# Performance work log

Measured on AMD Instinct MI355X. Metric: run time of the kernel, lower is better.

Reference implementation:

```python
import jax, jax.numpy as jnp
import numpy as np

B, N, HID = 2, 2048, 1024
NH = 16
HD = HID // NH

def setup_inputs() -> dict:
    key = jax.random.key(0)
    ks = jax.random.split(key, 5)
    s = 0.02
    return {
        "hidden_states": jax.random.normal(ks[0], (B, N, HID), jnp.float32),
        "attention_mask": jnp.zeros((B, 1, 1, N), jnp.float32),
        "Wq": jax.random.normal(ks[1], (HID, HID), jnp.float32) * s,
        "bq": jnp.zeros((HID,), jnp.float32),
        "Wk": jax.random.normal(ks[2], (HID, HID), jnp.float32) * s,
        "bk": jnp.zeros((HID,), jnp.float32),
        "Wv": jax.random.normal(ks[3], (HID, HID), jnp.float32) * s,
        "bv": jnp.zeros((HID,), jnp.float32),
    }

def reference(hidden_states, attention_mask, Wq, bq, Wk, bk, Wv, bv):
    b, n, _ = hidden_states.shape
    def split_heads(t):  # [b,n,hid] -> [b,h,n,d]
        return t.reshape(b, n, NH, HD).transpose(0, 2, 1, 3)
    q = split_heads(hidden_states @ Wq.T + bq)
    k = split_heads(hidden_states @ Wk.T + bk)
    v = split_heads(hidden_states @ Wv.T + bv)
    scores = jnp.einsum('bhnd,bhmd->bhnm', q, k) / jnp.sqrt(jnp.float32(HD)).astype(q.dtype)
    scores = scores + attention_mask
    scores = jnp.maximum(scores, jnp.finfo(scores.dtype).min)
    probs = jax.nn.softmax(scores, axis=-1)
    out = jnp.einsum('bhnm,bhmd->bhnd', probs, v)
    return out.transpose(0, 2, 1, 3).reshape(b, n, NH * HD)
```

## Files before the change

kernel.cpp:

```cpp
#include <hip/hip_runtime.h>

typedef unsigned short u16;
typedef unsigned int   u32;
typedef __attribute__((ext_vector_type(8))) short bf16x8;
typedef __attribute__((ext_vector_type(4))) float f32x4;
typedef __attribute__((ext_vector_type(2))) unsigned int u32x2;

__device__ __forceinline__ float bf2f(u16 u) { return __uint_as_float(((u32)u) << 16); }
__device__ __forceinline__ u16 f2bf(float f) {
    return (u16)((__float_as_uint(f) + 0x8000u) >> 16);
}
__device__ __forceinline__ u32 cvt_pk_bf16(float lo, float hi) {
    u32 r;
    asm("v_cvt_pk_bf16_f32 %0, %1, %2" : "=v"(r) : "v"(lo), "v"(hi));
    return r;
}
__device__ __forceinline__ void gload16(const void* g, void* l) {
    __builtin_amdgcn_global_load_lds((const __attribute__((address_space(1))) void*)g,
                                     (__attribute__((address_space(3))) void*)l, 16, 0, 0);
}
#define VMCNT(n) asm volatile("s_waitcnt vmcnt(" #n ")" ::: "memory")

struct us4 { u16 x, y, z, w; };
__global__ void cvt_all(const float* __restrict__ hs, const float* __restrict__ wq,
                        const float* __restrict__ wk, const float* __restrict__ wv,
                        u16* __restrict__ dst)
{
    int i = blockIdx.x * blockDim.x + threadIdx.x;
    const int stride = gridDim.x * blockDim.x;
    us4* d4 = (us4*)dst;
    for (; i < 1835008; i += stride) {
        const float4* s4;
        int j = i;
        if (j < 1048576)      { s4 = (const float4*)hs; }
        else if (j < 1310720) { s4 = (const float4*)wq; j -= 1048576; }
        else if (j < 1572864) { s4 = (const float4*)wk; j -= 1310720; }
        else                  { s4 = (const float4*)wv; j -= 1572864; }
        float4 v = s4[j];
        us4 o;
        o.x = f2bf(v.x); o.y = f2bf(v.y); o.z = f2bf(v.z); o.w = f2bf(v.w);
        d4[i] = o;
    }
}

__global__ __launch_bounds__(256) void qkv_gemm(
    const u16* __restrict__ hs,
    const u16* __restrict__ Wq, const u16* __restrict__ Wk, const u16* __restrict__ Wv,
    const float* __restrict__ bq, const float* __restrict__ bk, const float* __restrict__ bv,
    u16* __restrict__ oq, u16* __restrict__ ok, u16* __restrict__ ovt)
{
    __shared__ u16 smem[18432];
    u16* sA = smem;
    u16* sB = smem + 8192;

    const int tid  = threadIdx.x;
    const int lane = tid & 63;
    const int w    = tid >> 6;
    const int c15  = lane & 15;
    const int q4   = lane >> 4;
    const int mat  = blockIdx.x >> 3;
    const int cb   = blockIdx.x & 7;
    const int rb   = blockIdx.y;
    const int wr   = w >> 1, wc = w & 1;

    const u16*   W    = (mat == 0) ? Wq : (mat == 1 ? Wk : Wv);
    const float* bias = (mat == 0) ? bq : (mat == 1 ? bk : bv);

    f32x4 acc[4][4] = {};

    const int rs = tid >> 3;
    const int cs = ((tid & 7) ^ (rs & 7)) * 8;
    const u16* gA = hs + (rb * 128) * 1024;
    const u16* gB = W + (cb * 128) * 1024;

    for (int kb = 0; kb < 1024; kb += 64) {
        __syncthreads();
#pragma unroll
        for (int p = 0; p < 4; ++p)
            gload16(gA + (rs + 32 * p) * 1024 + kb + cs, sA + p * 2048 + w * 512);
#pragma unroll
        for (int p = 0; p < 4; ++p)
            gload16(gB + (rs + 32 * p) * 1024 + kb + cs, sB + p * 2048 + w * 512);
        __syncthreads();

#pragma unroll
        for (int kk = 0; kk < 2; ++kk) {
            const int cpos = ((kk * 4 + q4) ^ (c15 & 7)) * 8;
            bf16x8 af[4], bf[4];
#pragma unroll
            for (int mt = 0; mt < 4; ++mt)
                af[mt] = *(const bf16x8*)(sA + (wr * 64 + mt * 16 + c15) * 64 + cpos);
#pragma unroll
            for (int nt = 0; nt < 4; ++nt)
                bf[nt] = *(const bf16x8*)(sB + (wc * 64 + nt * 16 + c15) * 64 + cpos);
#pragma unroll
            for (int mt = 0; mt < 4; ++mt)
#pragma unroll
                for (int nt = 0; nt < 4; ++nt)
                    acc[mt][nt] = __builtin_amdgcn_mfma_f32_16x16x32_bf16(
                        af[mt], bf[nt], acc[mt][nt], 0, 0, 0);
        }
    }

    __syncthreads();
    const int h = cb * 2 + wc;
    float bvv[4];
#pragma unroll
    for (int nt = 0; nt < 4; ++nt)
        bvv[nt] = bias[cb * 128 + wc * 64 + nt * 16 + c15];

    u16* sc = smem + w * 4608;
    if (mat != 2) {
        u16* dst = (mat == 0) ? oq : ok;
#pragma unroll
        for (int mt = 0; mt < 4; ++mt)
#pragma unroll
            for (int nt = 0; nt < 4; ++nt)
#pragma unroll
                for (int rr = 0; rr < 4; ++rr)
                    sc[(mt * 16 + q4 * 4 + rr) * 72 + nt * 16 + c15] =
                        f2bf(acc[mt][nt][rr] + bvv[nt]);
#pragma unroll
        for (int p = 0; p < 8; ++p) {
            const int s = p * 64 + lane;
            const int rl = s >> 3, oct = (s & 7) * 8;
            bf16x8 vv = *(const bf16x8*)(sc + rl * 72 + oct);
            const int n = rb * 128 + wr * 64 + rl;
            const int bb = n >> 11, nn = n & 2047;
            *(bf16x8*)(dst + (((bb * 16 + h) * 2048) + nn) * 64 + oct) = vv;
        }
    } else {
#pragma unroll
        for (int mt = 0; mt < 4; ++mt)
#pragma unroll
            for (int nt = 0; nt < 4; ++nt)
#pragma unroll
                for (int rr = 0; rr < 4; ++rr)
                    sc[(nt * 16 + c15) * 72 + mt * 16 + q4 * 4 + rr] =
                        f2bf(acc[mt][nt][rr] + bvv[nt]);
#pragma unroll
        for (int p = 0; p < 8; ++p) {
            const int s = p * 64 + lane;
            const int dr = s >> 3, noct = (s & 7) * 8;
            bf16x8 vv = *(const bf16x8*)(sc + dr * 72 + noct);
            const int n0 = rb * 128 + wr * 64 + noct;
            const int bb = n0 >> 11, nn = n0 & 2047;
            *(bf16x8*)(ovt + ((bb * 16 + h) * 64 + dr) * 2048 + nn) = vv;
        }
    }
}

__global__ __launch_bounds__(256, 2) void attn(
    const u16* __restrict__ qm, const u16* __restrict__ km, const u16* __restrict__ vtm,
    const float* __restrict__ mask, float* __restrict__ out)
{
    __shared__ u16 sK0[8192];
    __shared__ u16 sV0[8192];
    __shared__ u16 sK1[8192];
    __shared__ u16 sV1[8192];

    const int tid = threadIdx.x, lane = tid & 63, w = tid >> 6;
    const int c15 = lane & 15, q4 = lane >> 4;
    const int bh = blockIdx.x;
    const int qt = blockIdx.y;
    const int b = bh >> 4;

    bf16x8 qf[2][2];
    const u16* qbase = qm + (bh * 2048 + qt * 128 + w * 32) * 64;
#pragma unroll
    for (int rt = 0; rt < 2; ++rt)
#pragma unroll
        for (int kt = 0; kt < 2; ++kt)
            qf[rt][kt] = *(const bf16x8*)(qbase + (rt * 16 + c15) * 64 + kt * 32 + q4 * 8);

    float l_acc[2] = {0.f, 0.f};
    f32x4 accO[2][4] = {};

    const u16* kbase  = km  + bh * 2048 * 64;
    const u16* vtbase = vtm + bh * 64 * 2048;

    const int rK   = tid >> 3;
    const int colK = ((tid & 7) ^ (rK & 7)) * 8;
    const int prK  = (rK & 3) | ((rK & 0x0C) << 1) | ((rK & 0x10) >> 2);
    const int rV   = tid >> 4;
    const int colV = ((tid & 15) ^ (rV & 7)) * 8;
    const int ldsW = w * 512;

    const float* mbase = mask + b * 2048 + 8 * q4;

    auto stage = [&](u16* dK, u16* dV, int TT) {
        const u16* kg = kbase + TT * 128 * 64;
        const u16* vg = vtbase + TT * 128;
#pragma unroll
        for (int p = 0; p < 4; ++p)
            gload16(kg + (prK + 32 * p) * 64 + colK, dK + p * 2048 + ldsW);
#pragma unroll
        for (int p = 0; p < 4; ++p)
            gload16(vg + (rV + 16 * p) * 2048 + colV, dV + p * 2048 + ldsW);
    };

    auto compute64 = [&](const u16* sKh, const u16* sVb, int pcBase, int kb) {
        float mkv[4][4];
#pragma unroll
        for (int t = 0; t < 4; ++t) {
            float4 m4 = *(const float4*)(mbase + kb + 32 * (t >> 1) + 4 * (t & 1));
            mkv[t][0] = m4.x * 1.4426950408889634f;
            mkv[t][1] = m4.y * 1.4426950408889634f;
            mkv[t][2] = m4.z * 1.4426950408889634f;
            mkv[t][3] = m4.w * 1.4426950408889634f;
        }

        f32x4 accST[4][2] = {};
        __builtin_amdgcn_s_setprio(1);
#pragma unroll
        for (int kt = 0; kt < 2; ++kt) {
            bf16x8 kf[4];
#pragma unroll
            for (int t = 0; t < 4; ++t) {
                const int cpos = (kt * 4 + q4) ^ (c15 & 7);
                kf[t] = *(const bf16x8*)(sKh + (t * 16 + c15) * 64 + cpos * 8);
            }
#pragma unroll
            for (int t = 0; t < 4; ++t)
#pragma unroll
                for (int rt = 0; rt < 2; ++rt)
                    accST[t][rt] = __builtin_amdgcn_mfma_f32_16x16x32_bf16(
                        kf[t], qf[rt][kt], accST[t][rt], 0, 0, 0);
        }
        __builtin_amdgcn_s_setprio(0);

        u32 pu[4][2][2];
#pragma unroll
        for (int t = 0; t < 4; ++t)
#pragma unroll
            for (int rt = 0; rt < 2; ++rt) {
                float p[4];
#pragma unroll
                for (int rr = 0; rr < 4; ++rr) {
                    p[rr] = __builtin_amdgcn_exp2f(
                        fmaf(accST[t][rt][rr], 0.18033688011112042f, mkv[t][rr]));
                    l_acc[rt] += p[rr];
                }
                pu[t][rt][0] = cvt_pk_bf16(p[0], p[1]);
                pu[t][rt][1] = cvt_pk_bf16(p[2], p[3]);
            }

        __builtin_amdgcn_s_setprio(1);
#pragma unroll
        for (int g = 0; g < 2; ++g) {
            bf16x8 vB[4];
#pragma unroll
            for (int nt = 0; nt < 4; ++nt) {
                const int d = nt * 16 + c15;
                const int pc = pcBase + ((4 * g + q4) ^ (d & 7));
                vB[nt] = *(const bf16x8*)(sVb + d * 128 + pc * 8);
            }
#pragma unroll
            for (int rt = 0; rt < 2; ++rt) {
                union { bf16x8 v; u32 u[4]; } ta;
                ta.u[0] = pu[2 * g][rt][0];
                ta.u[1] = pu[2 * g][rt][1];
                ta.u[2] = pu[2 * g + 1][rt][0];
                ta.u[3] = pu[2 * g + 1][rt][1];
#pragma unroll
                for (int nt = 0; nt < 4; ++nt)
                    accO[rt][nt] = __builtin_amdgcn_mfma_f32_16x16x32_bf16(
                        ta.v, vB[nt], accO[rt][nt], 0, 0, 0);
            }
        }
        __builtin_amdgcn_s_setprio(0);
    };

    stage(sK0, sV0, 0);
    stage(sK1, sV1, 1);

#pragma unroll 1
    for (int T = 0; T < 14; T += 2) {
        VMCNT(8);
        __builtin_amdgcn_s_barrier();
        __builtin_amdgcn_sched_barrier(0);
        compute64(sK0, sV0, 0, T * 128);
        compute64(sK0 + 64 * 64, sV0, 8, T * 128 + 64);
        __builtin_amdgcn_s_barrier();
        __builtin_amdgcn_sched_barrier(0);
        stage(sK0, sV0, T + 2);

        VMCNT(8);
        __builtin_amdgcn_s_barrier();
        __builtin_amdgcn_sched_barrier(0);
        compute64(sK1, sV1, 0, (T + 1) * 128);
        compute64(sK1 + 64 * 64, sV1, 8, (T + 1) * 128 + 64);
        __builtin_amdgcn_s_barrier();
        __builtin_amdgcn_sched_barrier(0);
        stage(sK1, sV1, T + 3);
    }
    VMCNT(8);
    __builtin_amdgcn_s_barrier();
    __builtin_amdgcn_sched_barrier(0);
    compute64(sK0, sV0, 0, 14 * 128);
    compute64(sK0 + 64 * 64, sV0, 8, 14 * 128 + 64);
    VMCNT(0);
    __builtin_amdgcn_s_barrier();
    __builtin_amdgcn_sched_barrier(0);
    compute64(sK1, sV1, 0, 15 * 128);
    compute64(sK1 + 64 * 64, sV1, 8, 15 * 128 + 64);

#pragma unroll
    for (int rt = 0; rt < 2; ++rt) {
        l_acc[rt] += __shfl_xor(l_acc[rt], 16);
        l_acc[rt] += __shfl_xor(l_acc[rt], 32);
    }

    const int h = bh & 15;
#pragma unroll
    for (int rt = 0; rt < 2; ++rt) {
        float inv[4];
#pragma unroll
        for (int rr = 0; rr < 4; ++rr)
            inv[rr] = 1.0f / __shfl(l_acc[rt], q4 * 4 + rr);
#pragma unroll
        for (int nt = 0; nt < 4; ++nt)
#pragma unroll
            for (int rr = 0; rr < 4; ++rr) {
                const int qrow = qt * 128 + w * 32 + rt * 16 + q4 * 4 + rr;
                const int d = nt * 16 + c15;
                out[(b * 2048 + qrow) * 1024 + h * 64 + d] = accO[rt][nt][rr] * inv[rr];
            }
    }
}

extern "C" void kernel_launch(void* const* d_in, const int* in_sizes, int n_in,
                              void* d_out, int out_size, void* d_ws, size_t ws_size,
                              hipStream_t stream)
{
    const float* hs   = (const float*)d_in[0];
    const float* mask = (const float*)d_in[1];
    const float* Wq   = (const float*)d_in[2];
    const float* bq   = (const float*)d_in[3];
    const float* Wk   = (const float*)d_in[4];
    const float* bk   = (const float*)d_in[5];
    const float* Wv   = (const float*)d_in[6];
    const float* bv   = (const float*)d_in[7];

    u16* ws   = (u16*)d_ws;
    u16* qw   = ws;
    u16* kw   = ws + 4194304;
    u16* vtw  = ws + 8388608;
    u16* hsb  = ws + 12582912;
    u16* wqb  = ws + 16777216;
    u16* wkb  = ws + 17825792;
    u16* wvb  = ws + 18874368;

    cvt_all<<<1024, 256, 0, stream>>>(hs, Wq, Wk, Wv, hsb);

    qkv_gemm<<<dim3(24, 32), 256, 0, stream>>>(hsb, wqb, wkb, wvb, bq, bk, bv, qw, kw, vtw);
    attn<<<dim3(32, 16), 256, 0, stream>>>(qw, kw, vtw, mask, (float*)d_out);
}
```

Measured before the change: 178.4 us.

## Double-buffer QKV GEMM LDS tiles with direct-to-LDS prefetch pipeline

Measured after the change: 162.3 us. -9.0%, faster.

```diff
diff --git a/kernel.cpp b/kernel.cpp
--- a/kernel.cpp
+++ b/kernel.cpp
@@ -49,9 +49,11 @@
     const float* __restrict__ bq, const float* __restrict__ bk, const float* __restrict__ bv,
     u16* __restrict__ oq, u16* __restrict__ ok, u16* __restrict__ ovt)
 {
-    __shared__ u16 smem[18432];
-    u16* sA = smem;
-    u16* sB = smem + 8192;
+    __shared__ u16 smem[32768];
+    u16* sA0 = smem;
+    u16* sB0 = smem + 8192;
+    u16* sA1 = smem + 16384;
+    u16* sB1 = smem + 24576;
 
     const int tid  = threadIdx.x;
     const int lane = tid & 63;
@@ -73,16 +75,17 @@
     const u16* gA = hs + (rb * 128) * 1024;
     const u16* gB = W + (cb * 128) * 1024;
 
-    for (int kb = 0; kb < 1024; kb += 64) {
-        __syncthreads();
+    auto stageQ = [&](u16* dA, u16* dB, int kb) {
 #pragma unroll
         for (int p = 0; p < 4; ++p)
-            gload16(gA + (rs + 32 * p) * 1024 + kb + cs, sA + p * 2048 + w * 512);
+            gload16(gA + (rs + 32 * p) * 1024 + kb + cs, dA + p * 2048 + w * 512);
 #pragma unroll
         for (int p = 0; p < 4; ++p)
-            gload16(gB + (rs + 32 * p) * 1024 + kb + cs, sB + p * 2048 + w * 512);
-        __syncthreads();
-
+            gload16(gB + (rs + 32 * p) * 1024 + kb + cs, dB + p * 2048 + w * 512);
+    };
+
+    auto computeQ = [&](const u16* sA, const u16* sB) {
+        __builtin_amdgcn_s_setprio(1);
 #pragma unroll
         for (int kk = 0; kk < 2; ++kk) {
             const int cpos = ((kk * 4 + q4) ^ (c15 & 7)) * 8;
@@ -100,7 +103,38 @@
                     acc[mt][nt] = __builtin_amdgcn_mfma_f32_16x16x32_bf16(
                         af[mt], bf[nt], acc[mt][nt], 0, 0, 0);
         }
-    }
+        __builtin_amdgcn_s_setprio(0);
+    };
+
+    stageQ(sA0, sB0, 0);
+    stageQ(sA1, sB1, 64);
+
+#pragma unroll 1
+    for (int T = 0; T < 14; T += 2) {
+        VMCNT(8);
+        __builtin_amdgcn_s_barrier();
+        __builtin_amdgcn_sched_barrier(0);
+        computeQ(sA0, sB0);
+        __builtin_amdgcn_s_barrier();
+        __builtin_amdgcn_sched_barrier(0);
+        stageQ(sA0, sB0, (T + 2) * 64);
+
+        VMCNT(8);
+        __builtin_amdgcn_s_barrier();
+        __builtin_amdgcn_sched_barrier(0);
+        computeQ(sA1, sB1);
+        __builtin_amdgcn_s_barrier();
+        __builtin_amdgcn_sched_barrier(0);
+        stageQ(sA1, sB1, (T + 3) * 64);
+    }
+    VMCNT(8);
+    __builtin_amdgcn_s_barrier();
+    __builtin_amdgcn_sched_barrier(0);
+    computeQ(sA0, sB0);
+    VMCNT(0);
+    __builtin_amdgcn_s_barrier();
+    __builtin_amdgcn_sched_barrier(0);
+    computeQ(sA1, sB1);
 
     __syncthreads();
     const int h = cb * 2 + wc;
```
